# Performance work log

Measured on AMD Instinct MI355X. Metric: run time of the kernel, lower is better.

The kernel has to match this reference:

```python
import jax, jax.numpy as jnp
import numpy as np

# hyperparameters (match init_kwargs)
LS = 0.2; GAMMA = 2.0; THING_W = 2.0; L_DB = 0.1; SIGMA = 0.05; TEMP = 0.1
L_DISTILL = 1.0; L_BPL = 0.5; L_ALIGN = 5.0; L_PROTO = 0.5; L_ENT = 0.3
L_IU = 0.5; L_IB = 0.5
MIN_PIX = 25; NUM_IDS = 24  # instance ids in [0, NUM_IDS)


def setup_inputs() -> dict:
    key = jax.random.key(0)
    k0, k1, k2, k3, k4 = jax.random.split(key, 5)
    B, C, H, W, D = 4, 27, 160, 160, 768
    return {
        "logits": jax.random.normal(k0, (B, C, H, W), jnp.float32),
        "cause_logits": jax.random.normal(k1, (B, C, H, W), jnp.float32),
        "dinov2_features": jax.random.normal(k2, (B, D, H, W), jnp.float32),
        "depth": jax.random.uniform(k3, (B, 1, H, W), jnp.float32),
        "instance_map": jax.random.randint(k4, (B, 1, H, W), 0, NUM_IDS),
    }


def _bce(x, y):
    x = jnp.clip(x, 1e-6, 1.0 - 1e-6)
    return -(y * jnp.log(x) + (1.0 - y) * jnp.log1p(-x)).mean()


def _forward(logits, cause_logits, dinov2_features, depth, instance_map):
    B, C, H, W = logits.shape
    logp = jax.nn.log_softmax(logits, axis=1)
    probs = jnp.exp(logp)

    # ---- distill: label-smoothed CE vs CAUSE hard labels, focal + thing + depth-boundary weights
    cause_labels = jnp.argmax(cause_logits, axis=1)  # (B,H,W)
    nll = -jnp.take_along_axis(logp, cause_labels[:, None], axis=1)[:, 0]  # (B,H,W)
    ce = (1.0 - LS) * nll + LS * (-logp.mean(axis=1))
    pt = jnp.exp(-jax.lax.stop_gradient(ce))
    w = (1.0 - pt) ** GAMMA
    thing = (cause_labels >= 11) & (cause_labels <= 18)
    w = jnp.where(thing, w * THING_W, w)
    gh = jnp.pad(jnp.abs(depth[:, :, 1:, :] - depth[:, :, :-1, :]), ((0, 0), (0, 0), (0, 1), (0, 0)))
    gw = jnp.pad(jnp.abs(depth[:, :, :, 1:] - depth[:, :, :, :-1]), ((0, 0), (0, 0), (0, 0), (0, 1)))
    gmag = (gh + gw)[:, 0]  # (B,H,W)
    gnorm = gmag / (gmag.mean() + 1e-6)
    w = w * (1.0 + L_DB * jnp.minimum(gnorm, 3.0))
    l_distill = (ce * w).mean()

    # ---- boundary preservation loss (CE re-weighted at pseudo-label boundaries)
    pl = jnp.pad(cause_labels, ((0, 0), (1, 1), (1, 1)), mode="edge")
    boundary = ((cause_labels != pl[:, 1:-1, 2:]) | (cause_labels != pl[:, 1:-1, :-2]) |
                (cause_labels != pl[:, 2:, 1:-1]) | (cause_labels != pl[:, :-2, 1:-1])).astype(jnp.float32)
    bsum = boundary.sum()
    l_bpl = jnp.where(bsum > 0, (ce * boundary).sum() / jnp.maximum(bsum, 1.0), 0.0)

    # ---- depth-boundary alignment
    two_s2 = 2.0 * SIGMA ** 2
    ddh = jnp.abs(depth[:, :, :, 1:] - depth[:, :, :, :-1])
    wh = jnp.exp(-(ddh ** 2) / two_s2)
    pdh = ((probs[:, :, :, 1:] - probs[:, :, :, :-1]) ** 2).sum(axis=1, keepdims=True)
    ddv = jnp.abs(depth[:, :, 1:, :] - depth[:, :, :-1, :])
    wv = jnp.exp(-(ddv ** 2) / two_s2)
    pdv = ((probs[:, :, 1:, :] - probs[:, :, :-1, :]) ** 2).sum(axis=1, keepdims=True)
    l_align = (wh * pdh).mean() + (wv * pdv).mean()

    # ---- feature prototype loss
    N = H * W
    probs_t = jax.nn.softmax(logits / TEMP, axis=1).reshape(B, C, N)   # (B,C,N)
    feats = dinov2_features.reshape(B, -1, N)                          # (B,D,N)
    protos = jnp.einsum("bdn,bcn->bdc", feats, probs_t)               # (B,D,C)
    wsum = probs_t.sum(axis=2)[:, None, :]                             # (B,1,C)
    protos = protos / (wsum + 1e-6)
    protos_n = protos / jnp.maximum(jnp.linalg.norm(protos, axis=1, keepdims=True), 1e-12)
    feats_n = feats / jnp.maximum(jnp.linalg.norm(feats, axis=1, keepdims=True), 1e-12)
    sim = jnp.einsum("bdc,bdn->bcn", protos_n, feats_n)               # (B,C,N)
    l_proto = -(probs_t * sim).sum() / (B * N)

    # ---- entropy loss
    l_ent = -(probs * logp).sum(axis=1).mean()

    # ---- instance boundary loss
    dh = jnp.abs(probs[:, :, 1:, :] - probs[:, :, :-1, :]).max(axis=1)
    dw = jnp.abs(probs[:, :, :, 1:] - probs[:, :, :, :-1]).max(axis=1)
    inst = instance_map[:, 0].astype(jnp.float32)
    th = (inst[:, 1:, :] != inst[:, :-1, :]).astype(jnp.float32)
    tw = (inst[:, :, 1:] != inst[:, :, :-1]).astype(jnp.float32)
    l_ib = (_bce(dh, th) + _bce(dw, tw)) / 2.0

    # ---- instance uniformity loss (vectorized segment reduce over instance ids)
    ids = instance_map[:, 0].reshape(B, N)                             # (B,N) int
    onehot = (ids[:, :, None] == jnp.arange(NUM_IDS)[None, None, :]).astype(jnp.float32)  # (B,N,K)
    counts = onehot.sum(axis=1)                                        # (B,K)
    pf = probs.reshape(B, C, N)
    s1 = jnp.einsum("bcn,bnk->bkc", pf, onehot)                       # per-id sum of probs
    s2 = jnp.einsum("bcn,bnk->bkc", pf * pf, onehot)                  # per-id sum of probs^2
    nc = jnp.maximum(counts, 1.0)[:, :, None]
    var = (s2 / nc - (s1 / nc) ** 2).mean(axis=2)                     # (B,K): mean over C of within-id variance
    valid = ((jnp.arange(NUM_IDS)[None, :] > 0) & (counts >= MIN_PIX)).astype(jnp.float32)
    l_iu = (var * valid).sum() / jnp.maximum(valid.sum(), 1.0)

    total = (L_DISTILL * l_distill + L_BPL * l_bpl + L_ALIGN * l_align +
             L_PROTO * l_proto + L_ENT * l_ent + L_IU * l_iu + L_IB * l_ib)
    return total


def reference(logits, cause_logits, dinov2_features, depth, instance_map):
    return _forward(logits, cause_logits, dinov2_features, depth, instance_map)
```

## Files before the change

kernel.cpp:

```cpp
#include <hip/hip_runtime.h>
#include <cstdint>
#include <cstddef>

#define BN 4
#define CC 27
#define HH 160
#define WW 160
#define HWp (HH*WW)
#define NPIX (BN*HWp)
#define DD 768
#define KK 24
#define NT 400
#define NTS 20
#define NSP 20
#define NPH (NTS/2)
#define GEMMB (BN*6*NSP)
#define TAILB (NPIX/256)

#define OFF_ACC 0
#define OFF_S1 32
#define OFF_S2 (OFF_S1+2592)
#define OFF_CNT (OFF_S2+2592)
#define ZERO_N (OFF_CNT+96)
#define OFF_NSQ8 ZERO_N
#define OFF_LAB (OFF_NSQ8 + 8*NPIX)
#define OFF_CE (OFF_LAB + NPIX/4)
#define OFF_PROBS (OFF_CE + NPIX)
#define OFF_PP (OFF_PROBS + BN*CC*HWp/2)
#define OFF_QP (OFF_PP + NSP*BN*CC*DD)
#define OFF_FBF (OFF_QP + NSP*BN*CC*DD)
#define OFF_WBF (OFF_FBF + (size_t)BN*6*NT*8192/4)

typedef __attribute__((ext_vector_type(4))) float f32x4;

__device__ __forceinline__ float wave_sum(float v) {
#pragma unroll
  for (int o = 32; o > 0; o >>= 1) v += __shfl_down(v, o, 64);
  return v;
}

__device__ __forceinline__ unsigned char f2fp8(float x) {
  return (unsigned char)(__builtin_amdgcn_cvt_pk_fp8_f32(x, x, 0, false) & 0xff);
}
__device__ __forceinline__ unsigned short f2bf(float x) {
  unsigned u = __builtin_bit_cast(unsigned, x);
  unsigned r = u + 0x7FFFu + ((u >> 16) & 1u);
  return (unsigned short)(r >> 16);
}
__device__ __forceinline__ float bf2f(unsigned short u) {
  unsigned v = ((unsigned)u) << 16;
  return __builtin_bit_cast(float, v);
}

__global__ void __launch_bounds__(256) k_big(const float* __restrict__ feats,
        const float* __restrict__ logits, const float* __restrict__ cause,
        const float* __restrict__ depth,
        unsigned char* __restrict__ fbf, float* __restrict__ nsq8,
        unsigned char* __restrict__ lab, float* __restrict__ ce_arr,
        unsigned short* __restrict__ probs, unsigned char* __restrict__ wbf,
        float* __restrict__ acc) {
  int t = threadIdx.x;
  if (blockIdx.x < 400) {
    int fcid = blockIdx.x;
    int slab = fcid % 50;
    int y = fcid / 50;
    int i = slab * 2048 + 8 * t;
    int b = i / HWp, r = i % HWp;
    int T = r >> 6, chunk = (r & 63) >> 3;
    const float* src0 = feats + ((size_t)b * DD + y * 96) * HWp + r;
    float n[8] = {0,0,0,0,0,0,0,0};
#pragma unroll 4
    for (int d = 0; d < 96; ++d) {
      int dgl = y * 96 + d;
      const float* src = src0 + (size_t)d * HWp;
      float4 v0 = *(const float4*)src;
      float4 v1 = *(const float4*)(src + 4);
      n[0]+=v0.x*v0.x; n[1]+=v0.y*v0.y; n[2]+=v0.z*v0.z; n[3]+=v0.w*v0.w;
      n[4]+=v1.x*v1.x; n[5]+=v1.y*v1.y; n[6]+=v1.z*v1.z; n[7]+=v1.w*v1.w;
      int pk0 = __builtin_amdgcn_cvt_pk_fp8_f32(v0.x, v0.y, 0, false);
      pk0 = __builtin_amdgcn_cvt_pk_fp8_f32(v0.z, v0.w, pk0, true);
      int pk1 = __builtin_amdgcn_cvt_pk_fp8_f32(v1.x, v1.y, 0, false);
      pk1 = __builtin_amdgcn_cvt_pk_fp8_f32(v1.z, v1.w, pk1, true);
      int dt = dgl >> 7, rin = dgl & 127;
      size_t addr = ((size_t)(b * 6 + dt) * NT + T) * 8192 + rin * 64
                  + ((chunk ^ (rin & 7)) * 8);
      int2 pk = make_int2(pk0, pk1);
      *(int2*)&fbf[addr] = pk;
    }
    float* nq = nsq8 + (size_t)y * NPIX + i;
    *(float4*)nq = make_float4(n[0], n[1], n[2], n[3]);
    *(float4*)(nq + 4) = make_float4(n[4], n[5], n[6], n[7]);
  } else {
    int i = (blockIdx.x - 400) * 256 + t;
    int b = i / HWp, r = i % HWp, h = r / WW, w = r % WW;
    float x[CC];
    {
      const float* cp = cause + (size_t)b * CC * HWp + r;
      float best = -1e30f; int bi = 0;
#pragma unroll
      for (int c = 0; c < CC; ++c) {
        float v = cp[(size_t)c * HWp];
        if (v > best) { best = v; bi = c; }
      }
      lab[i] = (unsigned char)bi;
      const float* lg = logits + (size_t)b * CC * HWp + r;
      float m = -1e30f;
#pragma unroll
      for (int c = 0; c < CC; ++c) { x[c] = lg[(size_t)c * HWp]; m = fmaxf(m, x[c]); }
      float sx = 0.f, xl = 0.f;
#pragma unroll
      for (int c = 0; c < CC; ++c) { sx += x[c]; if (c == bi) xl = x[c]; }
      float se = 0.f, set = 0.f, u = 0.f;
#pragma unroll
      for (int c = 0; c < CC; ++c) {
        float tc = x[c] - m;
        float e = expf(tc);
        se += e; u += e * tc;
        float e2 = e * e, e4 = e2 * e2;
        set += e4 * e4 * e2;
        x[c] = e;
      }
      float lse = logf(se);
      float inv_se = 1.f / se, inv_set = 1.f / set;
      float ent = lse - u * inv_se;
      unsigned short* pb = probs + (size_t)b * CC * HWp + r;
      int T = r >> 6, j = r & 63;
      unsigned char* wb = wbf + ((size_t)b * NT + T) * 4096;
#pragma unroll
      for (int c = 0; c < CC; ++c) {
        float e = x[c];
        pb[(size_t)c * HWp] = f2bf(e * inv_se);
        float e2 = e * e, e4 = e2 * e2;
        float ptc = (e4 * e4 * e2) * inv_set;
        wb[c * 64 + (((j >> 3) ^ (c & 7)) * 8) + (j & 7)] = f2fp8(ptc);
      }
      float ce = 0.8f * (m + lse - xl) + 0.2f * (m + lse - sx * (1.f / CC));
      ce_arr[i] = ce;
      const float* dp = depth + b * HWp;
      float d0 = dp[r];
      float gh = (h < HH-1) ? fabsf(dp[r+WW] - d0) : 0.f;
      float gw = (w < WW-1) ? fabsf(dp[r+1] - d0) : 0.f;
      float g = gh + gw;
      __shared__ float red[2];
      if (t < 2) red[t] = 0.f;
      __syncthreads();
      g = wave_sum(g); float es = wave_sum(ent);
      if ((t & 63) == 0) { atomicAdd(&red[0], g); atomicAdd(&red[1], es); }
      __syncthreads();
      if (t == 0) { atomicAdd(&acc[0], red[0]); atomicAdd(&acc[4], red[1]); }
    }
  }
}

__global__ void __launch_bounds__(256) k_mainB(const float* __restrict__ nsq8,
        unsigned char* __restrict__ wbf) {
  int t = threadIdx.x;
  int tt = blockIdx.x * 4 + (t >> 6);
  int j = t & 63;
  int b = tt / NT, T = tt % NT;
  int i = b * HWp + T * 64 + j;
  float ns = 0.f;
#pragma unroll
  for (int y = 0; y < 8; ++y) ns += nsq8[(size_t)y * NPIX + i];
  float invn = 1.f / fmaxf(sqrtf(ns), 1e-12f);
  unsigned char* wb = wbf + ((size_t)b * NT + T) * 4096;
#pragma unroll
  for (int c = 0; c < CC; ++c) {
    int a1 = c * 64 + ((((j >> 3) ^ (c & 7))) * 8) + (j & 7);
    float f = __builtin_amdgcn_cvt_f32_fp8((int)wb[a1], 0);
    wb[a1 + 32 * 64] = f2fp8(f * invn);
  }
}

__global__ void __launch_bounds__(256) k_gemmtail(const unsigned char* __restrict__ fbf,
        const unsigned char* __restrict__ wbf,
        float* __restrict__ Pp, float* __restrict__ Qp,
        const unsigned short* __restrict__ probs, const float* __restrict__ depth,
        const int* __restrict__ inst, const unsigned char* __restrict__ lab,
        const float* __restrict__ ce_arr, float* __restrict__ acc,
        float* __restrict__ s1g, float* __restrict__ s2g, float* __restrict__ cntg) {
  __shared__ __align__(16) unsigned char smem[49152];
  int t = threadIdx.x;
  if (blockIdx.x < GEMMB) {
    unsigned char (*As)[2][8192] = (unsigned char (*)[2][8192])smem;
    unsigned char (*Ws)[2][4096] = (unsigned char (*)[2][4096])(smem + 32768);
    int orig = blockIdx.x;
    int bx = (orig & 7) * 60 + (orig >> 3);
    int s  = bx % NSP;
    int dt = (bx / NSP) % 6;
    int b  = bx / (NSP * 6);
    int wave = t >> 6, lane = t & 63;
    int g = lane >> 4, rr = lane & 15;
    f32x4 acc4[2][4] = {};
    const unsigned char* Abase = fbf + ((size_t)(b*6+dt)*NT + s*NTS) * 8192;
    const unsigned char* Wbase = wbf + ((size_t)b*NT + s*NTS) * 4096;

#define STAGE2(ph, bufi) do { \
    _Pragma("unroll") \
    for (int c2_ = 0; c2_ < 2; ++c2_) { \
      const unsigned char* as_ = Abase + (size_t)((ph)*2 + c2_) * 8192; \
      const unsigned char* ws_ = Wbase + (size_t)((ph)*2 + c2_) * 4096; \
      _Pragma("unroll") \
      for (int i_ = 0; i_ < 2; ++i_) { \
        int off_ = wave*2048 + i_*1024; \
        __builtin_amdgcn_global_load_lds( \
          (const __attribute__((address_space(1))) void*)(as_ + off_ + lane*16), \
          (__attribute__((address_space(3))) void*)&As[bufi][c2_][off_], 16, 0, 0); \
      } \
      { \
        int off_ = wave*1024; \
        __builtin_amdgcn_global_load_lds( \
          (const __attribute__((address_space(1))) void*)(ws_ + off_ + lane*16), \
          (__attribute__((address_space(3))) void*)&Ws[bufi][c2_][off_], 16, 0, 0); \
      } \
    } \
  } while (0)

    STAGE2(0, 0);
    int cur = 0;
    for (int ph = 0; ph < NPH; ++ph) {
      if (ph + 1 < NPH) {
        STAGE2(ph + 1, cur ^ 1);
        asm volatile("s_waitcnt vmcnt(6)" ::: "memory");
      } else {
        asm volatile("s_waitcnt vmcnt(0)" ::: "memory");
      }
      __builtin_amdgcn_s_barrier();
      __builtin_amdgcn_sched_barrier(0);
#pragma unroll
      for (int c2 = 0; c2 < 2; ++c2) {
#pragma unroll
        for (int ks = 0; ks < 2; ++ks) {
          long a[2]; long wf[4];
#pragma unroll
          for (int dd = 0; dd < 2; ++dd) {
            int row = (wave*2 + dd)*16 + rr;
            int ck = (ks*4 + g) ^ (row & 7);
            a[dd] = *(const long*)&As[cur][c2][row*64 + ck*8];
          }
#pragma unroll
          for (int ct = 0; ct < 4; ++ct) {
            int row = ct*16 + rr;
            int ck = (ks*4 + g) ^ (row & 7);
            wf[ct] = *(const long*)&Ws[cur][c2][row*64 + ck*8];
          }
#pragma unroll
          for (int dd = 0; dd < 2; ++dd)
#pragma unroll
            for (int ct = 0; ct < 4; ++ct)
              acc4[dd][ct] = __builtin_amdgcn_mfma_f32_16x16x32_fp8_fp8(a[dd], wf[ct], acc4[dd][ct], 0, 0, 0);
        }
      }
      __builtin_amdgcn_sched_barrier(0);
      __builtin_amdgcn_s_barrier();
      cur ^= 1;
    }
#undef STAGE2
#pragma unroll
    for (int dd = 0; dd < 2; ++dd) {
#pragma unroll
      for (int ct = 0; ct < 4; ++ct) {
        int cp = ct * 16 + rr;
        int d = dt * 128 + (wave * 2 + dd) * 16 + g * 4;
        f32x4 v = acc4[dd][ct];
        if (cp < CC)
          *(f32x4*)&Pp[(((size_t)s * BN + b) * CC + cp) * DD + d] = v;
        else if (cp >= 32 && cp < 32 + CC)
          *(f32x4*)&Qp[(((size_t)s * BN + b) * CC + (cp - 32)) * DD + d] = v;
      }
    }
  } else {
    float* ls1 = (float*)smem;
    float* ls2 = ls1 + 4*KK*CC;
    float* lc  = ls2 + 4*KK*CC;
    float* red = lc + 4*KK;
    int wv = t >> 6;
    for (int idx = t; idx < 4*KK*CC; idx += 256) { ls1[idx] = 0.f; ls2[idx] = 0.f; }
    if (t < 4*KK) lc[t] = 0.f;
    if (t < 7) red[t] = 0.f;
    __syncthreads();
    int i = (blockIdx.x - GEMMB) * 256 + t;
    int b = i / HWp, r = i % HWp, h = r / WW, w = r % WW;
    const unsigned short* P = probs + (size_t)b * CC * HWp + r;
    const int* ip = inst + b * HWp;
    int id = ip[r];
    atomicAdd(&lc[wv*KK + id], 1.f);
    bool hasR = (w < WW-1), hasD = (h < HH-1);
    float sh = 0.f, sv = 0.f, mh = 0.f, mw = 0.f;
#pragma unroll
    for (int c = 0; c < CC; ++c) {
      float p  = bf2f(P[(size_t)c * HWp]);
      atomicAdd(&ls1[(wv*KK + id)*CC + c], p);
      atomicAdd(&ls2[(wv*KK + id)*CC + c], p * p);
      float pr = hasR ? bf2f(P[(size_t)c * HWp + 1])  : p;
      float pd = hasD ? bf2f(P[(size_t)c * HWp + WW]) : p;
      float dr = pr - p, dd = pd - p;
      sh += dr * dr; sv += dd * dd;
      mw = fmaxf(mw, fabsf(dr)); mh = fmaxf(mh, fabsf(dd));
    }
    const float* dp = depth + b * HWp;
    float d0 = dp[r];
    float aH = 0.f, aV = 0.f, bh = 0.f, bw = 0.f;
    float gh = 0.f, gw = 0.f;
    if (hasR) {
      float ddh = dp[r+1] - d0;
      gw = fabsf(ddh);
      aH = expf(-(ddh*ddh) * 200.f) * sh;
      float y = (ip[r+1] != ip[r]) ? 1.f : 0.f;
      float xx = fminf(fmaxf(mw, 1e-6f), 1.f - 1e-6f);
      bw = -(y * logf(xx) + (1.f - y) * log1pf(-xx));
    }
    if (hasD) {
      float ddv = dp[r+WW] - d0;
      gh = fabsf(ddv);
      aV = expf(-(ddv*ddv) * 200.f) * sv;
      float y = (ip[r+WW] != ip[r]) ? 1.f : 0.f;
      float xx = fminf(fmaxf(mh, 1e-6f), 1.f - 1e-6f);
      bh = -(y * logf(xx) + (1.f - y) * log1pf(-xx));
    }
    float ce = ce_arr[i];
    int l = lab[i];
    float ptf = expf(-ce);
    float wgt = (1.f - ptf) * (1.f - ptf);
    if (l >= 11 && l <= 18) wgt *= 2.f;
    float gmean = acc[0] * (1.f / NPIX);
    float gnorm = (gh + gw) / (gmean + 1e-6f);
    wgt *= 1.f + 0.1f * fminf(gnorm, 3.f);
    const unsigned char* lb = lab + b * HWp;
    int lL = lb[h*WW + (w>0 ? w-1 : w)];
    int lR = lb[h*WW + (w<WW-1 ? w+1 : w)];
    int lU = lb[(h>0 ? h-1 : h)*WW + w];
    int lD = lb[(h<HH-1 ? h+1 : h)*WW + w];
    float bnd = ((l != lL) | (l != lR) | (l != lU) | (l != lD)) ? 1.f : 0.f;
    float c_dist = ce * wgt, c_bnum = ce * bnd, c_bcnt = bnd;
    __syncthreads();
    aH = wave_sum(aH); aV = wave_sum(aV); bh = wave_sum(bh); bw = wave_sum(bw);
    c_dist = wave_sum(c_dist); c_bnum = wave_sum(c_bnum); c_bcnt = wave_sum(c_bcnt);
    if ((t & 63) == 0) {
      atomicAdd(&red[0], aH); atomicAdd(&red[1], aV);
      atomicAdd(&red[2], bh); atomicAdd(&red[3], bw);
      atomicAdd(&red[4], c_dist); atomicAdd(&red[5], c_bnum); atomicAdd(&red[6], c_bcnt);
    }
    __syncthreads();
    if (t == 0) {
      atomicAdd(&acc[5], red[0]); atomicAdd(&acc[6], red[1]);
      atomicAdd(&acc[7], red[2]); atomicAdd(&acc[8], red[3]);
      atomicAdd(&acc[1], red[4]); atomicAdd(&acc[2], red[5]); atomicAdd(&acc[3], red[6]);
    }
    for (int idx = t; idx < KK*CC; idx += 256) {
      atomicAdd(&s1g[b*KK*CC + idx], ls1[idx]+ls1[KK*CC+idx]+ls1[2*KK*CC+idx]+ls1[3*KK*CC+idx]);
      atomicAdd(&s2g[b*KK*CC + idx], ls2[idx]+ls2[KK*CC+idx]+ls2[2*KK*CC+idx]+ls2[3*KK*CC+idx]);
    }
    if (t < KK) atomicAdd(&cntg[b*KK + t], lc[t]+lc[KK+t]+lc[2*KK+t]+lc[3*KK+t]);
  }
}

__global__ void k_pfinal(const float* __restrict__ Pp, const float* __restrict__ Qp,
                         float* __restrict__ acc) {
  int bc = blockIdx.x;
  int b = bc / CC, c = bc % CC;
  float dot = 0.f, nsq = 0.f;
  for (int d = threadIdx.x; d < DD; d += 256) {
    float p = 0.f, q = 0.f;
#pragma unroll
    for (int s = 0; s < NSP; ++s) {
      size_t off = (((size_t)s * BN + b) * CC + c) * DD + d;
      p += Pp[off]; q += Qp[off];
    }
    dot += p * q; nsq += p * p;
  }
  __shared__ float red[2];
  if (threadIdx.x < 2) red[threadIdx.x] = 0.f;
  __syncthreads();
  dot = wave_sum(dot); nsq = wave_sum(nsq);
  if ((threadIdx.x & 63) == 0) { atomicAdd(&red[0], dot); atomicAdd(&red[1], nsq); }
  __syncthreads();
  if (threadIdx.x == 0) atomicAdd(&acc[9], red[0] / fmaxf(sqrtf(red[1]), 1e-12f));
}

__global__ void k_final(const float* __restrict__ s1g, const float* __restrict__ s2g,
                        const float* __restrict__ cntg, const float* __restrict__ acc,
                        float* __restrict__ out) {
  int t = threadIdx.x;
  float vsum = 0.f, vcnt = 0.f;
  if (t < BN*KK) {
    int k = t % KK;
    float count = cntg[t];
    float nc = fmaxf(count, 1.f);
    float var = 0.f;
#pragma unroll
    for (int c = 0; c < CC; ++c) {
      float m1 = s1g[t*CC + c] / nc;
      var += s2g[t*CC + c] / nc - m1 * m1;
    }
    var *= (1.f / CC);
    if (k > 0 && count >= 25.f) { vsum = var; vcnt = 1.f; }
  }
  __shared__ float red[2];
  if (t < 2) red[t] = 0.f;
  __syncthreads();
  vsum = wave_sum(vsum); vcnt = wave_sum(vcnt);
  if ((t & 63) == 0) { atomicAdd(&red[0], vsum); atomicAdd(&red[1], vcnt); }
  __syncthreads();
  if (t == 0) {
    float l_distill = acc[1] * (1.f / NPIX);
    float bcnt = acc[3];
    float l_bpl = (bcnt > 0.f) ? acc[2] / fmaxf(bcnt, 1.f) : 0.f;
    float l_align = acc[5] * (1.f / (BN*HH*(WW-1))) + acc[6] * (1.f / (BN*(HH-1)*WW));
    float l_ent = acc[4] * (1.f / NPIX);
    float l_ib = 0.5f * (acc[7] * (1.f / (BN*(HH-1)*WW)) + acc[8] * (1.f / (BN*HH*(WW-1))));
    float l_proto = -acc[9] * (1.f / NPIX);
    float l_iu = red[0] / fmaxf(red[1], 1.f);
    out[0] = 1.0f*l_distill + 0.5f*l_bpl + 5.0f*l_align + 0.5f*l_proto +
             0.3f*l_ent + 0.5f*l_iu + 0.5f*l_ib;
  }
}

extern "C" void kernel_launch(void* const* d_in, const int* in_sizes, int n_in,
                              void* d_out, int out_size, void* d_ws, size_t ws_size,
                              hipStream_t stream) {
  (void)in_sizes; (void)n_in; (void)out_size; (void)ws_size;
  const float* logits = (const float*)d_in[0];
  const float* cause  = (const float*)d_in[1];
  const float* feats  = (const float*)d_in[2];
  const float* depth  = (const float*)d_in[3];
  const int*   inst   = (const int*)d_in[4];
  float* ws = (float*)d_ws;
  float* acc = ws + OFF_ACC;
  float* s1  = ws + OFF_S1;
  float* s2  = ws + OFF_S2;
  float* cnt = ws + OFF_CNT;
  float* nsq8 = ws + OFF_NSQ8;
  float* ce  = ws + OFF_CE;
  float* Pp  = ws + OFF_PP;
  float* Qp  = ws + OFF_QP;
  unsigned char* lab = (unsigned char*)(ws + OFF_LAB);
  unsigned short* probs = (unsigned short*)(ws + OFF_PROBS);
  unsigned char* fbf = (unsigned char*)(ws + OFF_FBF);
  unsigned char* wbf = (unsigned char*)(ws + OFF_WBF);
  float* out = (float*)d_out;

  hipMemsetAsync(ws, 0, (size_t)ZERO_N * 4, stream);
  k_big<<<800, 256, 0, stream>>>(feats, logits, cause, depth, fbf, nsq8, lab, ce,
                                 probs, wbf, acc);
  k_mainB<<<400, 256, 0, stream>>>(nsq8, wbf);
  k_gemmtail<<<GEMMB + TAILB, 256, 0, stream>>>(fbf, wbf, Pp, Qp, probs, depth, inst,
                                                lab, ce, acc, s1, s2, cnt);
  k_pfinal<<<BN * CC, 256, 0, stream>>>(Pp, Qp, acc);
  k_final<<<1, 256, 0, stream>>>(s1, s2, cnt, acc, out);
}
```

Before: 196.5 us.

## Load fp8 GEMM operands directly into registers with MFMA-friendly tile layout

```diff
diff --git a/kernel.cpp b/kernel.cpp
--- a/kernel.cpp
+++ b/kernel.cpp
@@ -13,7 +13,6 @@
 #define NT 400
 #define NTS 20
 #define NSP 20
-#define NPH (NTS/2)
 #define GEMMB (BN*6*NSP)
 #define TAILB (NPIX/256)
 
@@ -32,6 +31,9 @@
 #define OFF_WBF (OFF_FBF + (size_t)BN*6*NT*8192/4)
 
 typedef __attribute__((ext_vector_type(4))) float f32x4;
+typedef __attribute__((ext_vector_type(2))) long longx2;
+
+__device__ __forceinline__ int chunkpos(int c) { return (c & 3) * 16 + (c >> 2) * 8; }
 
 __device__ __forceinline__ float wave_sum(float v) {
 #pragma unroll
@@ -67,6 +69,7 @@
     int i = slab * 2048 + 8 * t;
     int b = i / HWp, r = i % HWp;
     int T = r >> 6, chunk = (r & 63) >> 3;
+    int pos = chunkpos(chunk);
     const float* src0 = feats + ((size_t)b * DD + y * 96) * HWp + r;
     float n[8] = {0,0,0,0,0,0,0,0};
 #pragma unroll 4
@@ -82,8 +85,7 @@
       int pk1 = __builtin_amdgcn_cvt_pk_fp8_f32(v1.x, v1.y, 0, false);
       pk1 = __builtin_amdgcn_cvt_pk_fp8_f32(v1.z, v1.w, pk1, true);
       int dt = dgl >> 7, rin = dgl & 127;
-      size_t addr = ((size_t)(b * 6 + dt) * NT + T) * 8192 + rin * 64
-                  + ((chunk ^ (rin & 7)) * 8);
+      size_t addr = ((size_t)(b * 6 + dt) * NT + T) * 8192 + rin * 64 + pos;
       int2 pk = make_int2(pk0, pk1);
       *(int2*)&fbf[addr] = pk;
     }
@@ -125,6 +127,7 @@
       float ent = lse - u * inv_se;
       unsigned short* pb = probs + (size_t)b * CC * HWp + r;
       int T = r >> 6, j = r & 63;
+      int pos = chunkpos(j >> 3) + (j & 7);
       unsigned char* wb = wbf + ((size_t)b * NT + T) * 4096;
 #pragma unroll
       for (int c = 0; c < CC; ++c) {
@@ -132,7 +135,7 @@
         pb[(size_t)c * HWp] = f2bf(e * inv_se);
         float e2 = e * e, e4 = e2 * e2;
         float ptc = (e4 * e4 * e2) * inv_set;
-        wb[c * 64 + (((j >> 3) ^ (c & 7)) * 8) + (j & 7)] = f2fp8(ptc);
+        wb[c * 64 + pos] = f2fp8(ptc);
       }
       float ce = 0.8f * (m + lse - xl) + 0.2f * (m + lse - sx * (1.f / CC));
       ce_arr[i] = ce;
@@ -164,9 +167,10 @@
   for (int y = 0; y < 8; ++y) ns += nsq8[(size_t)y * NPIX + i];
   float invn = 1.f / fmaxf(sqrtf(ns), 1e-12f);
   unsigned char* wb = wbf + ((size_t)b * NT + T) * 4096;
+  int pos = chunkpos(j >> 3) + (j & 7);
 #pragma unroll
   for (int c = 0; c < CC; ++c) {
-    int a1 = c * 64 + ((((j >> 3) ^ (c & 7))) * 8) + (j & 7);
+    int a1 = c * 64 + pos;
     float f = __builtin_amdgcn_cvt_f32_fp8((int)wb[a1], 0);
     wb[a1 + 32 * 64] = f2fp8(f * invn);
   }
@@ -179,11 +183,9 @@
         const int* __restrict__ inst, const unsigned char* __restrict__ lab,
         const float* __restrict__ ce_arr, float* __restrict__ acc,
         float* __restrict__ s1g, float* __restrict__ s2g, float* __restrict__ cntg) {
-  __shared__ __align__(16) unsigned char smem[49152];
+  __shared__ float tsm[4*KK*CC*2 + 4*KK + 8];
   int t = threadIdx.x;
   if (blockIdx.x < GEMMB) {
-    unsigned char (*As)[2][8192] = (unsigned char (*)[2][8192])smem;
-    unsigned char (*Ws)[2][4096] = (unsigned char (*)[2][4096])(smem + 32768);
     int orig = blockIdx.x;
     int bx = (orig & 7) * 60 + (orig >> 3);
     int s  = bx % NSP;
@@ -192,76 +194,46 @@
     int wave = t >> 6, lane = t & 63;
     int g = lane >> 4, rr = lane & 15;
     f32x4 acc4[2][4] = {};
-    const unsigned char* Abase = fbf + ((size_t)(b*6+dt)*NT + s*NTS) * 8192;
-    const unsigned char* Wbase = wbf + ((size_t)b*NT + s*NTS) * 4096;
-
-#define STAGE2(ph, bufi) do { \
-    _Pragma("unroll") \
-    for (int c2_ = 0; c2_ < 2; ++c2_) { \
-      const unsigned char* as_ = Abase + (size_t)((ph)*2 + c2_) * 8192; \
-      const unsigned char* ws_ = Wbase + (size_t)((ph)*2 + c2_) * 4096; \
-      _Pragma("unroll") \
-      for (int i_ = 0; i_ < 2; ++i_) { \
-        int off_ = wave*2048 + i_*1024; \
-        __builtin_amdgcn_global_load_lds( \
-          (const __attribute__((address_space(1))) void*)(as_ + off_ + lane*16), \
-          (__attribute__((address_space(3))) void*)&As[bufi][c2_][off_], 16, 0, 0); \
-      } \
-      { \
-        int off_ = wave*1024; \
-        __builtin_amdgcn_global_load_lds( \
-          (const __attribute__((address_space(1))) void*)(ws_ + off_ + lane*16), \
-          (__attribute__((address_space(3))) void*)&Ws[bufi][c2_][off_], 16, 0, 0); \
-      } \
-    } \
-  } while (0)
-
-    STAGE2(0, 0);
-    int cur = 0;
-    for (int ph = 0; ph < NPH; ++ph) {
-      if (ph + 1 < NPH) {
-        STAGE2(ph + 1, cur ^ 1);
-        asm volatile("s_waitcnt vmcnt(6)" ::: "memory");
-      } else {
-        asm volatile("s_waitcnt vmcnt(0)" ::: "memory");
+    const unsigned char* At = fbf + ((size_t)(b*6+dt)*NT + s*NTS) * 8192
+                             + (wave*32 + rr) * 64 + g*16;
+    const unsigned char* Wt = wbf + ((size_t)b*NT + s*NTS) * 4096 + rr*64 + g*16;
+    longx2 af[3][2], wf[3][4];
+#pragma unroll
+    for (int p = 0; p < 3; ++p) {
+#pragma unroll
+      for (int dd = 0; dd < 2; ++dd)
+        af[p][dd] = *(const longx2*)(At + (size_t)p*8192 + dd*1024);
+#pragma unroll
+      for (int ct = 0; ct < 4; ++ct)
+        wf[p][ct] = *(const longx2*)(Wt + (size_t)p*4096 + ct*1024);
+    }
+#pragma unroll
+    for (int tc = 0; tc < NTS; ++tc) {
+      const int sl = tc % 3;
+#pragma unroll
+      for (int dd = 0; dd < 2; ++dd)
+#pragma unroll
+        for (int ct = 0; ct < 4; ++ct) {
+          acc4[dd][ct] = __builtin_amdgcn_mfma_f32_16x16x32_fp8_fp8(
+              af[sl][dd].x, wf[sl][ct].x, acc4[dd][ct], 0, 0, 0);
+          acc4[dd][ct] = __builtin_amdgcn_mfma_f32_16x16x32_fp8_fp8(
+              af[sl][dd].y, wf[sl][ct].y, acc4[dd][ct], 0, 0, 0);
+        }
+      if (tc + 3 < NTS) {
+#pragma unroll
+        for (int dd = 0; dd < 2; ++dd)
+          af[sl][dd] = *(const longx2*)(At + (size_t)(tc+3)*8192 + dd*1024);
+#pragma unroll
+        for (int ct = 0; ct < 4; ++ct)
+          wf[sl][ct] = *(const longx2*)(Wt + (size_t)(tc+3)*4096 + ct*1024);
       }
-      __builtin_amdgcn_s_barrier();
-      __builtin_amdgcn_sched_barrier(0);
-#pragma unroll
-      for (int c2 = 0; c2 < 2; ++c2) {
-#pragma unroll
-        for (int ks = 0; ks < 2; ++ks) {
-          long a[2]; long wf[4];
-#pragma unroll
-          for (int dd = 0; dd < 2; ++dd) {
-            int row = (wave*2 + dd)*16 + rr;
-            int ck = (ks*4 + g) ^ (row & 7);
-            a[dd] = *(const long*)&As[cur][c2][row*64 + ck*8];
-          }
-#pragma unroll
-          for (int ct = 0; ct < 4; ++ct) {
-            int row = ct*16 + rr;
-            int ck = (ks*4 + g) ^ (row & 7);
-            wf[ct] = *(const long*)&Ws[cur][c2][row*64 + ck*8];
-          }
-#pragma unroll
-          for (int dd = 0; dd < 2; ++dd)
-#pragma unroll
-            for (int ct = 0; ct < 4; ++ct)
-              acc4[dd][ct] = __builtin_amdgcn_mfma_f32_16x16x32_fp8_fp8(a[dd], wf[ct], acc4[dd][ct], 0, 0, 0);
-        }
-      }
-      __builtin_amdgcn_sched_barrier(0);
-      __builtin_amdgcn_s_barrier();
-      cur ^= 1;
-    }
-#undef STAGE2
+    }
 #pragma unroll
     for (int dd = 0; dd < 2; ++dd) {
 #pragma unroll
       for (int ct = 0; ct < 4; ++ct) {
         int cp = ct * 16 + rr;
-        int d = dt * 128 + (wave * 2 + dd) * 16 + g * 4;
+        int d = dt * 128 + wave * 32 + dd * 16 + g * 4;
         f32x4 v = acc4[dd][ct];
         if (cp < CC)
           *(f32x4*)&Pp[(((size_t)s * BN + b) * CC + cp) * DD + d] = v;
@@ -270,7 +242,7 @@
       }
     }
   } else {
-    float* ls1 = (float*)smem;
+    float* ls1 = tsm;
     float* ls2 = ls1 + 4*KK*CC;
     float* lc  = ls2 + 4*KK*CC;
     float* red = lc + 4*KK;
```

New measurement: 198.5 us. Within noise of the previous version (+1.0%).
